# Performance work log

Measured on AMD Instinct MI355X. Metric: run time of the kernel, lower is better.

The kernel has to match this reference:

```python
import jax, jax.numpy as jnp
import numpy as np

AGENT_SIZE = 64
NEIGH_SIZE = 64
NUM_HEAD = 4
MID_SIZE = 32
N_AGENT = 200000
HM = NUM_HEAD * MID_SIZE  # 128
OUT = HM // 2             # 64


def _xavier(key, shape):
    fan_in, fan_out = shape[0], shape[1]
    std = (2.0 / (fan_in + fan_out)) ** 0.5
    return jax.random.normal(key, shape, dtype=jnp.float32) * std


def setup_inputs() -> dict:
    key = jax.random.key(0)
    ks = jax.random.split(key, 12)
    agent = jax.random.normal(ks[0], (N_AGENT, AGENT_SIZE), dtype=jnp.float32)
    neighbor = jax.random.normal(ks[1], (N_AGENT, 4, NEIGH_SIZE), dtype=jnp.float32)
    neighbor_mask = jax.random.randint(ks[2], (N_AGENT, 4), 0, 2, dtype=jnp.int32)
    return {
        "agent": agent,
        "neighbor": neighbor,
        "neighbor_mask": neighbor_mask,
        "W_agent": _xavier(ks[3], (AGENT_SIZE, HM)),
        "b_agent": jnp.zeros((HM,), jnp.float32),
        "W_neigh": _xavier(ks[4], (NEIGH_SIZE, HM)),
        "b_neigh": jnp.zeros((HM,), jnp.float32),
        "W_hid": _xavier(ks[5], (NEIGH_SIZE, HM)),
        "b_hid": jnp.zeros((HM,), jnp.float32),
        "W_out": _xavier(ks[6], (HM, OUT)),
        "b_out": jnp.zeros((OUT,), jnp.float32),
    }


def reference(agent, neighbor, neighbor_mask,
              W_agent, b_agent, W_neigh, b_neigh,
              W_hid, b_hid, W_out, b_out):
    n = agent.shape[0]
    mask = neighbor_mask.astype(jnp.float32)  # [n, 4], 1 = masked
    # linear + relu projections
    a = jax.nn.relu(agent @ W_agent + b_agent).reshape(n, NUM_HEAD, MID_SIZE)          # [n,h,m]
    nr = jax.nn.relu(neighbor @ W_neigh + b_neigh).reshape(n, 4, NUM_HEAD, MID_SIZE)   # [n,4,h,m]
    nh = jax.nn.relu(neighbor @ W_hid + b_hid).reshape(n, 4, NUM_HEAD, MID_SIZE)       # [n,4,h,m]
    # attention logits: agent . neighbor per head -> [n, h, 4]
    att = jnp.einsum('nhm,nkhm->nhk', a, nr)
    att_score = jax.nn.softmax(mask[:, None, :] * -1e8 + att, axis=-1)                 # [n,h,4]
    att_score = (1.0 - mask[:, None, :]) * att_score
    # weighted MEAN over the 4 neighbors (faithful to .mean(2))
    out = jnp.einsum('nhk,nkhm->nhm', att_score, nh) / 4.0                              # [n,h,m]
    out = out.reshape(n, HM)
    return jax.nn.relu(out @ W_out + b_out)
```

## Files before the change

kernel.cpp:

```cpp
#include <hip/hip_runtime.h>
#include <cstdint>


typedef _Float16 f16;
typedef f16 f16x8 __attribute__((ext_vector_type(8)));
typedef float f32x4 __attribute__((ext_vector_type(4)));

#define MFMA(a, b, c) __builtin_amdgcn_mfma_f32_16x16x32_f16(a, b, c, 0, 0, 0)

__device__ __forceinline__ f16x8 ld_cvt8(const float* __restrict__ p) {
    float4 a = *(const float4*)p;
    float4 b = *(const float4*)(p + 4);
    f16x8 r;
    r[0] = (f16)a.x; r[1] = (f16)a.y; r[2] = (f16)a.z; r[3] = (f16)a.w;
    r[4] = (f16)b.x; r[5] = (f16)b.y; r[6] = (f16)b.z; r[7] = (f16)b.w;
    return r;
}

__device__ __forceinline__ float rowsum16(float x) {
    x += __int_as_float(__builtin_amdgcn_update_dpp(0, __float_as_int(x), 0x128, 0xf, 0xf, true));
    x += __int_as_float(__builtin_amdgcn_update_dpp(0, __float_as_int(x), 0x124, 0xf, 0xf, true));
    x += __int_as_float(__builtin_amdgcn_update_dpp(0, __float_as_int(x), 0x122, 0xf, 0xf, true));
    x += __int_as_float(__builtin_amdgcn_update_dpp(0, __float_as_int(x), 0x121, 0xf, 0xf, true));
    return x;
}

__global__ void prep_w(const float* __restrict__ Wa, const float* __restrict__ Wn,
                       const float* __restrict__ Wh, const float* __restrict__ Wo,
                       f16* __restrict__ ws) {
    int i = blockIdx.x * 256 + threadIdx.x;
    int m = i >> 13;
    int j = i & 8191;
    if (m < 3) {
        const float* W = (m == 0) ? Wa : ((m == 1) ? Wn : Wh);
        int n = j >> 6, k = j & 63;
        ws[m * 8192 + j] = (f16)W[k * 128 + n];
    } else {
        int n = j >> 7, k = j & 127;
        ws[24576 + j] = (f16)Wo[k * 64 + n];
    }
}

__global__ __launch_bounds__(256, 2)
void gat_mfma(const float* __restrict__ agent,
              const float* __restrict__ neighbor,
              const int*   __restrict__ nmask,
              const f16*   __restrict__ ws,
              const float* __restrict__ ba, const float* __restrict__ bn,
              const float* __restrict__ bh, const float* __restrict__ bo,
              float* __restrict__ out)
{
    __shared__ float mneg[256];
    __shared__ f16   ot[64 * 136];

    const int tid  = threadIdx.x;
    const int lane = tid & 63;
    const int h    = __builtin_amdgcn_readfirstlane(tid >> 6);
    const int l15  = lane & 15;
    const int q    = lane >> 4;
    const long base = (long)blockIdx.x * 64;

    mneg[tid] = -1e8f * (float)nmask[base * 4 + tid];
    __syncthreads();

    const float bav[2] = { ba[h * 32 + l15], ba[h * 32 + 16 + l15] };
    const float bnv[2] = { bn[h * 32 + l15], bn[h * 32 + 16 + l15] };
    const float bhv[2] = { bh[h * 32 + l15], bh[h * 32 + 16 + l15] };
    const float bov    = bo[h * 16 + l15];

    const f16* wsn = ws + 8192;
    const f16* wsh = ws + 16384;
    const f16* wso = ws + 24576;

    f16x8 wn[2][2], wh[2][2];
    #pragma unroll
    for (int ct = 0; ct < 2; ++ct)
        #pragma unroll
        for (int ks = 0; ks < 2; ++ks) {
            int n = h * 32 + ct * 16 + l15;
            wn[ct][ks] = *(const f16x8*)(wsn + n * 64 + ks * 32 + q * 8);
            wh[ct][ks] = *(const f16x8*)(wsh + n * 64 + ks * 32 + q * 8);
        }

    f32x4 pa[4][2];
    {
        f16x8 wa[2][2];
        #pragma unroll
        for (int ct = 0; ct < 2; ++ct)
            #pragma unroll
            for (int ks = 0; ks < 2; ++ks)
                wa[ct][ks] = *(const f16x8*)(ws + (h * 32 + ct * 16 + l15) * 64 + ks * 32 + q * 8);
        #pragma unroll
        for (int rt = 0; rt < 4; ++rt) {
            f32x4 c0 = {0.f, 0.f, 0.f, 0.f}, c1 = {0.f, 0.f, 0.f, 0.f};
            const float* ap = agent + (base + rt * 16 + l15) * 64 + q * 8;
            f16x8 a0 = ld_cvt8(ap);
            f16x8 a1 = ld_cvt8(ap + 32);
            c0 = MFMA(a0, wa[0][0], c0); c0 = MFMA(a1, wa[0][1], c0);
            c1 = MFMA(a0, wa[1][0], c1); c1 = MFMA(a1, wa[1][1], c1);
            #pragma unroll
            for (int r = 0; r < 4; ++r) {
                c0[r] = fmaxf(c0[r] + bav[0], 0.f);
                c1[r] = fmaxf(c1[r] + bav[1], 0.f);
            }
            pa[rt][0] = c0; pa[rt][1] = c1;
        }
    }

    f32x4 oacc[4][2] = {};
    f32x4 lsum[4] = {};
    #pragma unroll
    for (int k = 0; k < 4; ++k) {
        #pragma unroll
        for (int rt = 0; rt < 4; ++rt) {
            const float* nb = neighbor + ((base + rt * 16 + l15) * 4 + k) * 64 + q * 8;
            f16x8 a0 = ld_cvt8(nb);
            f16x8 a1 = ld_cvt8(nb + 32);
            f32x4 n0 = {0.f,0.f,0.f,0.f}, n1 = {0.f,0.f,0.f,0.f};
            f32x4 h0 = {0.f,0.f,0.f,0.f}, h1 = {0.f,0.f,0.f,0.f};
            n0 = MFMA(a0, wn[0][0], n0); n0 = MFMA(a1, wn[0][1], n0);
            n1 = MFMA(a0, wn[1][0], n1); n1 = MFMA(a1, wn[1][1], n1);
            h0 = MFMA(a0, wh[0][0], h0); h0 = MFMA(a1, wh[0][1], h0);
            h1 = MFMA(a0, wh[1][0], h1); h1 = MFMA(a1, wh[1][1], h1);
            #pragma unroll
            for (int r = 0; r < 4; ++r) {
                n0[r] = fmaxf(n0[r] + bnv[0], 0.f);
                n1[r] = fmaxf(n1[r] + bnv[1], 0.f);
                h0[r] = fmaxf(h0[r] + bhv[0], 0.f);
                h1[r] = fmaxf(h1[r] + bhv[1], 0.f);
            }
            #pragma unroll
            for (int r = 0; r < 4; ++r) {
                float tp = pa[rt][0][r] * n0[r] + pa[rt][1][r] * n1[r];
                float logit = rowsum16(tp);
                float s = logit + mneg[(rt * 16 + q * 4 + r) * 4 + k];
                float e = __expf(s);
                lsum[rt][r] += e;
                float ep = (s > -1e7f) ? e : 0.f;
                oacc[rt][0][r] += ep * h0[r];
                oacc[rt][1][r] += ep * h1[r];
            }
        }
    }

    #pragma unroll
    for (int rt = 0; rt < 4; ++rt)
        #pragma unroll
        for (int r = 0; r < 4; ++r) {
            float inv = 0.25f / (lsum[rt][r] + 1e-30f);
            int row = rt * 16 + q * 4 + r;
            ot[row * 136 + h * 32 + l15]      = (f16)(oacc[rt][0][r] * inv);
            ot[row * 136 + h * 32 + 16 + l15] = (f16)(oacc[rt][1][r] * inv);
        }
    __syncthreads();

    f16x8 wof[4];
    #pragma unroll
    for (int ks = 0; ks < 4; ++ks)
        wof[ks] = *(const f16x8*)(wso + (h * 16 + l15) * 128 + ks * 32 + q * 8);
    #pragma unroll
    for (int rt = 0; rt < 4; ++rt) {
        f32x4 y = {0.f, 0.f, 0.f, 0.f};
        #pragma unroll
        for (int ks = 0; ks < 4; ++ks) {
            f16x8 of = *(const f16x8*)(ot + (rt * 16 + l15) * 136 + ks * 32 + q * 8);
            y = MFMA(of, wof[ks], y);
        }
        #pragma unroll
        for (int r = 0; r < 4; ++r)
            out[(base + rt * 16 + q * 4 + r) * 64 + h * 16 + l15] = fmaxf(y[r] + bov, 0.f);
    }
}

extern "C" void kernel_launch(void* const* d_in, const int* in_sizes, int n_in,
                              void* d_out, int out_size, void* d_ws, size_t ws_size,
                              hipStream_t stream) {
    const float* agent    = (const float*)d_in[0];
    const float* neighbor = (const float*)d_in[1];
    const int*   nmask    = (const int*)d_in[2];
    const float* Wa = (const float*)d_in[3];
    const float* ba = (const float*)d_in[4];
    const float* Wn = (const float*)d_in[5];
    const float* bn = (const float*)d_in[6];
    const float* Wh = (const float*)d_in[7];
    const float* bh = (const float*)d_in[8];
    const float* Wo = (const float*)d_in[9];
    const float* bo = (const float*)d_in[10];
    float* out = (float*)d_out;
    f16* ws = (f16*)d_ws;

    prep_w<<<128, 256, 0, stream>>>(Wa, Wn, Wh, Wo, ws);

    const int n = in_sizes[0] / 64;
    const int blocks = n / 64;
    gat_mfma<<<blocks, 256, 0, stream>>>(agent, neighbor, nmask, ws,
                                         ba, bn, bh, bo, out);
}
```

Baseline: 416.4 us.

## Restructure loop per row-tile to cut registers and raise occupancy

The kernel now processes each 16-row tile fully (agent projection, all four neighbors, normalization) inside a non-unrolled loop instead of holding all tiles' accumulators live at once. This shrinks live register state, so launch bounds are raised from 2 to 4 blocks per SIMD-group to increase occupancy and hide memory latency. The agent weights are reloaded per tile and loop-level memory parallelism within a wave is reduced, trading per-wave ILP for more waves. The mask-staging barrier is also moved after the weight loads.

```diff
diff --git a/kernel.cpp b/kernel.cpp
--- a/kernel.cpp
+++ b/kernel.cpp
@@ -41,7 +41,7 @@
     }
 }
 
-__global__ __launch_bounds__(256, 2)
+__global__ __launch_bounds__(256, 4)
 void gat_mfma(const float* __restrict__ agent,
               const float* __restrict__ neighbor,
               const int*   __restrict__ nmask,
@@ -61,7 +61,6 @@
     const long base = (long)blockIdx.x * 64;
 
     mneg[tid] = -1e8f * (float)nmask[base * 4 + tid];
-    __syncthreads();
 
     const float bav[2] = { ba[h * 32 + l15], ba[h * 32 + 16 + l15] };
     const float bnv[2] = { bn[h * 32 + l15], bn[h * 32 + 16 + l15] };
@@ -82,37 +81,35 @@
             wh[ct][ks] = *(const f16x8*)(wsh + n * 64 + ks * 32 + q * 8);
         }
 
-    f32x4 pa[4][2];
-    {
-        f16x8 wa[2][2];
-        #pragma unroll
-        for (int ct = 0; ct < 2; ++ct)
-            #pragma unroll
-            for (int ks = 0; ks < 2; ++ks)
-                wa[ct][ks] = *(const f16x8*)(ws + (h * 32 + ct * 16 + l15) * 64 + ks * 32 + q * 8);
-        #pragma unroll
-        for (int rt = 0; rt < 4; ++rt) {
-            f32x4 c0 = {0.f, 0.f, 0.f, 0.f}, c1 = {0.f, 0.f, 0.f, 0.f};
+    __syncthreads();
+
+    #pragma unroll 1
+    for (int rt = 0; rt < 4; ++rt) {
+        f32x4 p0 = {0.f, 0.f, 0.f, 0.f}, p1 = {0.f, 0.f, 0.f, 0.f};
+        {
             const float* ap = agent + (base + rt * 16 + l15) * 64 + q * 8;
             f16x8 a0 = ld_cvt8(ap);
             f16x8 a1 = ld_cvt8(ap + 32);
-            c0 = MFMA(a0, wa[0][0], c0); c0 = MFMA(a1, wa[0][1], c0);
-            c1 = MFMA(a0, wa[1][0], c1); c1 = MFMA(a1, wa[1][1], c1);
+            #pragma unroll
+            for (int ct = 0; ct < 2; ++ct) {
+                f16x8 w0 = *(const f16x8*)(ws + (h * 32 + ct * 16 + l15) * 64 + q * 8);
+                f16x8 w1 = *(const f16x8*)(ws + (h * 32 + ct * 16 + l15) * 64 + 32 + q * 8);
+                f32x4 c = {0.f, 0.f, 0.f, 0.f};
+                c = MFMA(a0, w0, c);
+                c = MFMA(a1, w1, c);
+                if (ct == 0) p0 = c; else p1 = c;
+            }
             #pragma unroll
             for (int r = 0; r < 4; ++r) {
-                c0[r] = fmaxf(c0[r] + bav[0], 0.f);
-                c1[r] = fmaxf(c1[r] + bav[1], 0.f);
+                p0[r] = fmaxf(p0[r] + bav[0], 0.f);
+                p1[r] = fmaxf(p1[r] + bav[1], 0.f);
             }
-            pa[rt][0] = c0; pa[rt][1] = c1;
         }
-    }
 
-    f32x4 oacc[4][2] = {};
-    f32x4 lsum[4] = {};
-    #pragma unroll
-    for (int k = 0; k < 4; ++k) {
+        f32x4 o0 = {0.f, 0.f, 0.f, 0.f}, o1 = {0.f, 0.f, 0.f, 0.f};
+        f32x4 ls = {0.f, 0.f, 0.f, 0.f};
         #pragma unroll
-        for (int rt = 0; rt < 4; ++rt) {
+        for (int k = 0; k < 4; ++k) {
             const float* nb = neighbor + ((base + rt * 16 + l15) * 4 + k) * 64 + q * 8;
             f16x8 a0 = ld_cvt8(nb);
             f16x8 a1 = ld_cvt8(nb + 32);
@@ -131,27 +128,25 @@
             }
             #pragma unroll
             for (int r = 0; r < 4; ++r) {
-                float tp = pa[rt][0][r] * n0[r] + pa[rt][1][r] * n1[r];
+                float tp = p0[r] * n0[r] + p1[r] * n1[r];
                 float logit = rowsum16(tp);
                 float s = logit + mneg[(rt * 16 + q * 4 + r) * 4 + k];
                 float e = __expf(s);
-                lsum[rt][r] += e;
+                ls[r] += e;
                 float ep = (s > -1e7f) ? e : 0.f;
-                oacc[rt][0][r] += ep * h0[r];
-                oacc[rt][1][r] += ep * h1[r];
+                o0[r] += ep * h0[r];
+                o1[r] += ep * h1[r];
             }
         }
-    }
 
-    #pragma unroll
-    for (int rt = 0; rt < 4; ++rt)
         #pragma unroll
         for (int r = 0; r < 4; ++r) {
-            float inv = 0.25f / (lsum[rt][r] + 1e-30f);
+            float inv = 0.25f / (ls[r] + 1e-30f);
             int row = rt * 16 + q * 4 + r;
-            ot[row * 136 + h * 32 + l15]      = (f16)(oacc[rt][0][r] * inv);
-            ot[row * 136 + h * 32 + 16 + l15] = (f16)(oacc[rt][1][r] * inv);
+            ot[row * 136 + h * 32 + l15]      = (f16)(o0[r] * inv);
+            ot[row * 136 + h * 32 + 16 + l15] = (f16)(o1[r] * inv);
         }
+    }
     __syncthreads();
 
     f16x8 wof[4];
```

Result: no change. 421.5 us (+1.2%).
